# Kernel tuning notes

Measured on AMD Instinct MI355X. Metric: run time of the kernel, lower is better.

Reference implementation:

```python
import jax, jax.numpy as jnp
import numpy as np

B = 256
NUM_IN_CAPS = 1152   # 6*6*32
NUM_OUT_CAPS = 10
VEC_IN = 8
VEC_OUT = 16
ROUTING_ITERS = 3


def squash(x, axis):
    # squash(v) = |v|^2/(1+|v|^2) * v/|v|  (matches torch module, no eps)
    mag_squ = jnp.sum(x * x, axis=axis, keepdims=True)
    return mag_squ / (1.0 + mag_squ) * (x / jnp.sqrt(mag_squ))


def setup_inputs() -> dict:
    key = jax.random.key(0)
    k = jax.random.split(key, 6)
    x = jax.random.normal(k[0], (B, 1, 28, 28), dtype=jnp.float32)
    conv1_w = jax.random.normal(k[1], (256, 1, 9, 9), dtype=jnp.float32) * 0.1
    conv1_b = jnp.zeros((256,), dtype=jnp.float32)
    pc_w = jax.random.normal(k[2], (256, 256, 9, 9), dtype=jnp.float32) * 0.02  # out = 32 caps * 8 dims
    pc_b = jnp.zeros((256,), dtype=jnp.float32)
    # routing transform W: original shape [1,1152,160,8,1] -> [1152,10,16,8]
    W = jax.random.normal(k[3], (NUM_IN_CAPS, NUM_OUT_CAPS, VEC_OUT, VEC_IN), dtype=jnp.float32)
    dc_bias = jnp.zeros((NUM_OUT_CAPS, VEC_OUT), dtype=jnp.float32)
    return {"x": x, "conv1_w": conv1_w, "conv1_b": conv1_b,
            "pc_w": pc_w, "pc_b": pc_b, "W": W, "dc_bias": dc_bias}


def _conv(x, w, b, stride):
    y = jax.lax.conv_general_dilated(x, w, (stride, stride), 'VALID',
                                     dimension_numbers=('NCHW', 'OIHW', 'NCHW'))
    return y + b[None, :, None, None]


def reference(x, conv1_w, conv1_b, pc_w, pc_b, W, dc_bias):
    # conv1: [B,1,28,28] -> [B,256,20,20]  (no activation in original module)
    h = _conv(x, conv1_w, conv1_b, stride=1)
    # primaryCaps conv: -> [B,256,6,6] -> [B,1152,8]
    caps = _conv(h, pc_w, pc_b, stride=2)
    caps = caps.reshape(caps.shape[0], -1, VEC_IN)          # [B,1152,8]
    caps = squash(caps, axis=-1)
    # u_hat[b,i,j,d] = sum_k W[i,j,d,k] * caps[b,i,k]  (the original broadcast-mul-sum)
    u_hat = jnp.einsum('ijdk,bik->bijd', W, caps)           # [B,1152,10,16]
    b_ij = jnp.zeros(u_hat.shape[:3], dtype=u_hat.dtype)    # [B,1152,10]
    for r in range(ROUTING_ITERS):
        c_ij = jax.nn.softmax(b_ij, axis=2)                 # softmax over output caps
        s_j = jnp.einsum('bij,bijd->bjd', c_ij, u_hat) + dc_bias  # [B,10,16]
        v_j = squash(s_j, axis=-1)
        if r != ROUTING_ITERS - 1:
            b_ij = b_ij + jnp.einsum('bijd,bjd->bij', u_hat, v_j)
    return v_j  # [B,10,16]
```

## Files before the change

kernel.cpp:

```cpp
#include <hip/hip_runtime.h>
#include <hip/hip_bf16.h>


typedef __attribute__((ext_vector_type(8))) short short8;
typedef __attribute__((ext_vector_type(4))) float float4v;

__global__ __launch_bounds__(640) void conv1_kernel(const float* __restrict__ x,
    const float* __restrict__ w, const float* __restrict__ bias,
    __hip_bfloat16* __restrict__ ht){
  __shared__ float img[784];
  __shared__ float wsv[32 * 81];
  __shared__ ushort tile[400 * 33];
  int b = blockIdx.x;
  int og = blockIdx.y;
  int t = threadIdx.x;
  const float* xb = x + (size_t)b * 784;
  for (int idx = t; idx < 784; idx += 640) img[idx] = xb[idx];
  for (int idx = t; idx < 2592; idx += 640) wsv[idx] = w[(size_t)og * 2592 + idx];
  __syncthreads();
  int o_l = t / 20;
  int y   = t - o_l * 20;
  float acc[20];
  #pragma unroll
  for (int i = 0; i < 20; i++) acc[i] = 0.f;
  #pragma unroll
  for (int r = 0; r < 9; r++){
    float row[28];
    const float4* rp = (const float4*)&img[(y + r) * 28];
    #pragma unroll
    for (int q = 0; q < 7; q++){
      float4 v4 = rp[q];
      row[4*q+0]=v4.x; row[4*q+1]=v4.y; row[4*q+2]=v4.z; row[4*q+3]=v4.w;
    }
    #pragma unroll
    for (int s = 0; s < 9; s++){
      float wv = wsv[o_l * 81 + r * 9 + s];
      #pragma unroll
      for (int xx = 0; xx < 20; xx++)
        acc[xx] = fmaf(wv, row[xx + s], acc[xx]);
    }
  }
  float bv = bias[og * 32 + o_l];
  #pragma unroll
  for (int xx = 0; xx < 20; xx++){
    __hip_bfloat16 hv = __float2bfloat16(acc[xx] + bv);
    tile[(y * 20 + xx) * 33 + o_l] = *(ushort*)&hv;
  }
  __syncthreads();
  __hip_bfloat16* hb = ht + (size_t)b * 102400 + og * 32;
  for (int idx = t; idx < 6400; idx += 640){
    int pos = idx >> 4, op = idx & 15;
    unsigned v = (unsigned)tile[pos * 33 + op * 2]
               | ((unsigned)tile[pos * 33 + op * 2 + 1] << 16);
    *(unsigned*)(hb + (size_t)pos * 256 + op * 2) = v;
  }
}

__global__ __launch_bounds__(256) void arepack_kernel(const float* __restrict__ w2,
    ushort* __restrict__ A2s){
  __shared__ float wbuf[64 * 81];
  int o = blockIdx.x;
  int t = threadIdx.x;
  int ow = o >> 6, fo = (o >> 4) & 3, l15 = o & 15;
  size_t obase8 = (size_t)ow * 165888 + (size_t)fo * 64 + (size_t)l15 * 4;
  for (int c0 = 0; c0 < 256; c0 += 64){
    __syncthreads();
    for (int idx = t; idx < 5184; idx += 256)
      wbuf[idx] = w2[(size_t)o * 20736 + (size_t)c0 * 81 + idx];
    __syncthreads();
    for (int idx = t; idx < 2592; idx += 256){
      int rs = idx >> 5;
      int cp = (idx & 31) * 2;
      int cg = c0 + cp;
      int ct = cg >> 5, quad = (cg >> 3) & 3, e = cg & 7;
      __hip_bfloat16 b0 = __float2bfloat16(wbuf[cp * 81 + rs]);
      __hip_bfloat16 b1 = __float2bfloat16(wbuf[(cp + 1) * 81 + rs]);
      unsigned pack = (unsigned)*(ushort*)&b0 | ((unsigned)*(ushort*)&b1 << 16);
      size_t si = (obase8 + (size_t)ct * 256 + (size_t)rs * 2048 + quad) * 8 + e;
      *(unsigned*)(A2s + si) = pack;
    }
  }
}

__global__ __launch_bounds__(256, 2) void conv2_mfma_kernel(
    const __hip_bfloat16* __restrict__ ht, const short8* __restrict__ A2,
    float* __restrict__ caps4){
  __shared__ ushort img[2][400 * 40];
  int bx  = blockIdx.x;
  int xcd = bx & 7;
  int kq  = xcd >> 1;
  int p   = ((bx >> 3) << 1) | (xcd & 1);
  int b0  = p * 2;
  int t = threadIdx.x;
  int lane = t & 63;
  int wid  = t >> 6;
  int l15  = lane & 15;
  int quad = lane >> 4;

  int bn[3], slc[3];
  #pragma unroll
  for (int fn = 0; fn < 3; fn++){
    int n = fn * 16 + l15;
    int y = n / 6, xx = n - y * 6;
    if (n >= 36){ y = 0; xx = 0; }
    bn[fn]  = 40 * y + 2 * xx;
    slc[fn] = (quad + 4 * y) % 5;
  }
  const short8* i0p = (const short8*)&img[0][0];
  const short8* i1p = (const short8*)&img[1][0];

  float4v acc[4][6];
  #pragma unroll
  for (int fo = 0; fo < 4; fo++)
    #pragma unroll
    for (int fn = 0; fn < 6; fn++)
      acc[fo][fn] = (float4v){0.f, 0.f, 0.f, 0.f};

  for (int ci = 0; ci < 2; ci++){
    int ct = kq * 2 + ci;
    __syncthreads();
    #pragma unroll
    for (int im = 0; im < 2; im++){
      const __hip_bfloat16* hb = ht + (size_t)(b0 + im) * 102400;
      for (int idx = t; idx < 1600; idx += 256){
        int pp = idx >> 2, q = idx & 3;
        int sl = (q + 2 * (pp / 20)) % 5;
        uint4 v = *(const uint4*)(hb + (size_t)pp * 256 + ct * 32 + q * 8);
        *(uint4*)&img[im][pp * 40 + sl * 8] = v;
      }
    }
    __syncthreads();

    const short8* ap = A2 + ((size_t)wid * 648 + ct) * 256 + l15 * 4 + quad;

    short8 aF[2][4], bF[2][6];
    #pragma unroll
    for (int fo = 0; fo < 4; fo++) aF[0][fo] = ap[fo * 64];
    #pragma unroll
    for (int fn = 0; fn < 6; fn++){
      int f3 = (fn < 3) ? fn : fn - 3;
      const short8* ib = (fn < 3) ? i0p : i1p;
      bF[0][fn] = ib[bn[f3] * 5 + slc[f3]];
    }

    int rn = 0, sn = 0, r2m = 0;
    #pragma unroll 2
    for (int rs = 0; rs < 81; rs++){
      int cur = rs & 1, nxt = cur ^ 1;
      sn++;
      if (sn == 9){ sn = 0; rn++; r2m += 2; if (r2m >= 5) r2m -= 5; }
      int nrs = (rs < 80) ? rs + 1 : 80;
      int roff = rn * 20 + sn;
      const short8* apn = ap + (size_t)nrs * 2048;
      #pragma unroll
      for (int fo = 0; fo < 4; fo++) aF[nxt][fo] = apn[fo * 64];
      #pragma unroll
      for (int fn = 0; fn < 6; fn++){
        int f3 = (fn < 3) ? fn : fn - 3;
        const short8* ib = (fn < 3) ? i0p : i1p;
        int sl = slc[f3] + r2m; if (sl >= 5) sl -= 5;
        bF[nxt][fn] = ib[(bn[f3] + roff) * 5 + sl];
      }
      #pragma unroll
      for (int fo = 0; fo < 4; fo++)
        #pragma unroll
        for (int fn = 0; fn < 6; fn++)
          acc[fo][fn] = __builtin_amdgcn_mfma_f32_16x16x32_bf16(aF[cur][fo], bF[cur][fn], acc[fo][fn], 0, 0, 0);
    }
  }

  #pragma unroll
  for (int fn = 0; fn < 6; fn++){
    int im = (fn < 3) ? 0 : 1;
    int f3 = (fn < 3) ? fn : fn - 3;
    int pos = f3 * 16 + l15;
    if (pos < 36){
      float* cb = caps4 + ((size_t)kq * 256 + b0 + im) * 9216;
      #pragma unroll
      for (int fo = 0; fo < 4; fo++){
        int ob = wid * 64 + fo * 16 + quad * 4;
        #pragma unroll
        for (int rr = 0; rr < 4; rr++)
          cb[(size_t)(ob + rr) * 36 + pos] = acc[fo][fn][rr];
      }
    }
  }
}

__global__ __launch_bounds__(256) void squash4_kernel(const float* __restrict__ caps4,
    const float* __restrict__ bias, float* __restrict__ caps){
  size_t cid = (size_t)blockIdx.x * 256 + threadIdx.x;
  size_t base = cid * 8;
  const size_t STR = 2359296;
  float4 a0 = *(const float4*)(caps4 + base);
  float4 a1 = *(const float4*)(caps4 + base + 4);
  #pragma unroll
  for (int k = 1; k < 4; k++){
    float4 q0 = *(const float4*)(caps4 + k * STR + base);
    float4 q1 = *(const float4*)(caps4 + k * STR + base + 4);
    a0.x+=q0.x; a0.y+=q0.y; a0.z+=q0.z; a0.w+=q0.w;
    a1.x+=q1.x; a1.y+=q1.y; a1.z+=q1.z; a1.w+=q1.w;
  }
  int off = (int)(base % 9216);
  float v[8] = {a0.x,a0.y,a0.z,a0.w,a1.x,a1.y,a1.z,a1.w};
  #pragma unroll
  for (int e = 0; e < 8; e++) v[e] += bias[(off + e) / 36];
  float msq = 0.f;
  #pragma unroll
  for (int e = 0; e < 8; e++) msq += v[e]*v[e];
  float scale = sqrtf(msq) / (1.f + msq);
  float* cp = caps + base;
  #pragma unroll
  for (int e = 0; e < 8; e++) cp[e] = v[e]*scale;
}

__global__ __launch_bounds__(256) void uhat_kernel(const float* __restrict__ caps,
    const float* __restrict__ Wt, __hip_bfloat16* __restrict__ uh){
  __shared__ float cl[4096];
  int i0 = blockIdx.x * 32;
  int b0 = blockIdx.y * 16;
  int t = threadIdx.x;
  for (int idx = t; idx < 4096; idx += 256){
    int b_l = idx >> 8;
    int rest = idx & 255;
    cl[idx] = caps[((size_t)(b0 + b_l) * 1152 + i0 + (rest >> 3)) * 8 + (rest & 7)];
  }
  __syncthreads();
  int wid = t >> 6, l = t & 63;
  for (int ii = 0; ii < 8; ii++){
    int i = i0 + ii * 4 + wid;
    float wreg[3][8];
    #pragma unroll
    for (int m = 0; m < 3; m++){
      int jd = m * 64 + l;
      if (jd < 160){
        const float4* wp = (const float4*)&Wt[((size_t)i * 160 + jd) * 8];
        float4 p0 = wp[0], p1 = wp[1];
        wreg[m][0]=p0.x; wreg[m][1]=p0.y; wreg[m][2]=p0.z; wreg[m][3]=p0.w;
        wreg[m][4]=p1.x; wreg[m][5]=p1.y; wreg[m][6]=p1.z; wreg[m][7]=p1.w;
      }
    }
    for (int b_l = 0; b_l < 16; b_l++){
      const float4* cp4 = (const float4*)&cl[(b_l * 32 + ii * 4 + wid) * 8];
      float4 ca = cp4[0], cb = cp4[1];
      float ck[8] = {ca.x, ca.y, ca.z, ca.w, cb.x, cb.y, cb.z, cb.w};
      size_t ubase = ((size_t)(b0 + b_l) * 1152 + i) * 160;
      #pragma unroll
      for (int m = 0; m < 3; m++){
        int jd = m * 64 + l;
        if (jd < 160){
          float uv = 0.f;
          #pragma unroll
          for (int k = 0; k < 8; k++) uv = fmaf(wreg[m][k], ck[k], uv);
          uh[ubase + jd] = __float2bfloat16(uv);
        }
      }
    }
  }
}

__global__ __launch_bounds__(640, 2) void route_kernel(
    const __hip_bfloat16* __restrict__ u, const float* __restrict__ vin,
    const float* __restrict__ dcb, float* __restrict__ bbuf,
    float* __restrict__ vout, int mode){
  __shared__ float vs[160];
  __shared__ float dotb[320];
  __shared__ float cl[320];
  __shared__ float sp[4][160];
  int b = blockIdx.x;
  int t = threadIdx.x;
  int ipar = t / 160;
  int jd   = t - ipar * 160;
  int j    = jd >> 4;
  if (mode && t < 160) vs[t] = vin[b * 160 + t];
  __syncthreads();
  const __hip_bfloat16* ub = u + (size_t)b * 184320;
  float sacc = 0.f;
  for (int ch = 0; ch < 36; ch++){
    int ibase = ch * 32 + ipar * 8;
    float ureg[8];
    #pragma unroll
    for (int ii = 0; ii < 8; ii++)
      ureg[ii] = __bfloat162float(ub[(size_t)(ibase + ii) * 160 + jd]);
    if (mode){
      #pragma unroll
      for (int ii = 0; ii < 8; ii++){
        float pp = ureg[ii] * vs[jd];
        pp += __shfl_xor(pp, 1, 16);
        pp += __shfl_xor(pp, 2, 16);
        pp += __shfl_xor(pp, 4, 16);
        pp += __shfl_xor(pp, 8, 16);
        if ((jd & 15) == 0) dotb[(ipar * 8 + ii) * 10 + j] = pp;
      }
      __syncthreads();
      if (t < 320){
        float val = dotb[t];
        float* bg = bbuf + (size_t)b * 11520 + ch * 320 + t;
        if (mode == 2) val += *bg;
        else *bg = val;
        dotb[t] = val;
      }
      __syncthreads();
      if (t < 32){
        float dv[10]; float mx = -1e30f;
        #pragma unroll
        for (int q = 0; q < 10; q++){ dv[q] = dotb[t * 10 + q]; mx = fmaxf(mx, dv[q]); }
        float se = 0.f;
        #pragma unroll
        for (int q = 0; q < 10; q++){ dv[q] = __expf(dv[q] - mx); se += dv[q]; }
        float inv = 1.f / se;
        #pragma unroll
        for (int q = 0; q < 10; q++) cl[t * 10 + q] = dv[q] * inv;
      }
      __syncthreads();
      #pragma unroll
      for (int ii = 0; ii < 8; ii++)
        sacc = fmaf(cl[(ipar * 8 + ii) * 10 + j], ureg[ii], sacc);
    } else {
      #pragma unroll
      for (int ii = 0; ii < 8; ii++) sacc += ureg[ii];
    }
  }
  if (!mode) sacc *= 0.1f;
  sp[ipar][jd] = sacc;
  __syncthreads();
  if (t < 160){
    float sv = sp[0][t] + sp[1][t] + sp[2][t] + sp[3][t] + dcb[t];
    float msq = sv * sv;
    msq += __shfl_xor(msq, 1, 16);
    msq += __shfl_xor(msq, 2, 16);
    msq += __shfl_xor(msq, 4, 16);
    msq += __shfl_xor(msq, 8, 16);
    float scale = sqrtf(msq) / (1.f + msq);
    vout[b * 160 + t] = sv * scale;
  }
}

extern "C" void kernel_launch(void* const* d_in, const int* in_sizes, int n_in,
                              void* d_out, int out_size, void* d_ws, size_t ws_size,
                              hipStream_t stream){
  (void)in_sizes; (void)n_in; (void)out_size; (void)ws_size;
  const float* x   = (const float*)d_in[0];
  const float* w1  = (const float*)d_in[1];
  const float* b1  = (const float*)d_in[2];
  const float* w2  = (const float*)d_in[3];
  const float* b2  = (const float*)d_in[4];
  const float* W   = (const float*)d_in[5];
  const float* dcb = (const float*)d_in[6];
  float* out = (float*)d_out;

  char* ws = (char*)d_ws;
  __hip_bfloat16* ht  = (__hip_bfloat16*)(ws);
  ushort* A2s  = (ushort*)(ws + 52428800);
  float* caps4 = (float*)(ws + 63045632);
  __hip_bfloat16* uh = (__hip_bfloat16*)(ws);
  float* caps = (float*)(ws + 100794368);
  float* bbuf = (float*)(ws + 110231552);
  float* vbuf = (float*)(ws + 122028032);

  conv1_kernel<<<dim3(256, 8), 640, 0, stream>>>(x, w1, b1, ht);
  arepack_kernel<<<256, 256, 0, stream>>>(w2, A2s);
  conv2_mfma_kernel<<<512, 256, 0, stream>>>(ht, (const short8*)A2s, caps4);
  squash4_kernel<<<1152, 256, 0, stream>>>(caps4, b2, caps);
  uhat_kernel<<<dim3(36, 16), 256, 0, stream>>>(caps, W, uh);
  route_kernel<<<256, 640, 0, stream>>>(uh, vbuf, dcb, bbuf, vbuf, 0);
  route_kernel<<<256, 640, 0, stream>>>(uh, vbuf, dcb, bbuf, vbuf, 1);
  route_kernel<<<256, 640, 0, stream>>>(uh, vbuf, dcb, bbuf, out, 2);
}
```

Baseline: 473.6 us.

## Fuse three routing passes into one kernel with transposed u_hat layout

Replaces the three per-iteration routing launches with a single kernel per batch element that holds the routing logits in registers and the coupling coefficients in LDS. This removes the global bbuf and vbuf round trips and two launches. u_hat is now written in a transposed [b][jd][i] layout, and a new repack kernel transposes W so the u_hat kernel reads it coalesced. The fused kernel uses large LDS (about 50KB) and 576 threads with one block per batch element, which may limit occupancy.

```diff
diff --git a/kernel.cpp b/kernel.cpp
--- a/kernel.cpp
+++ b/kernel.cpp
@@ -4,6 +4,8 @@
 
 typedef __attribute__((ext_vector_type(8))) short short8;
 typedef __attribute__((ext_vector_type(4))) float float4v;
+
+__device__ inline float bfu(ushort v){ return __uint_as_float((unsigned)v << 16); }
 
 __global__ __launch_bounds__(640) void conv1_kernel(const float* __restrict__ x,
     const float* __restrict__ w, const float* __restrict__ bias,
@@ -82,6 +84,19 @@
   }
 }
 
+__global__ __launch_bounds__(256) void wrepack_kernel(const float* __restrict__ W,
+    float* __restrict__ Wr){
+  __shared__ float tile[64][65];
+  int r0 = blockIdx.x * 64;
+  int c0 = blockIdx.y * 64;
+  int t = threadIdx.x; int lx = t & 63, ly = t >> 6;
+  for (int rr = ly; rr < 64; rr += 4)
+    tile[rr][lx] = W[(size_t)(r0 + rr) * 1280 + c0 + lx];
+  __syncthreads();
+  for (int rr = ly; rr < 64; rr += 4)
+    Wr[(size_t)(c0 + rr) * 1152 + r0 + lx] = tile[lx][rr];
+}
+
 __global__ __launch_bounds__(256, 2) void conv2_mfma_kernel(
     const __hip_bfloat16* __restrict__ ht, const short8* __restrict__ A2,
     float* __restrict__ caps4){
@@ -214,125 +229,118 @@
   for (int e = 0; e < 8; e++) cp[e] = v[e]*scale;
 }
 
-__global__ __launch_bounds__(256) void uhat_kernel(const float* __restrict__ caps,
-    const float* __restrict__ Wt, __hip_bfloat16* __restrict__ uh){
-  __shared__ float cl[4096];
-  int i0 = blockIdx.x * 32;
-  int b0 = blockIdx.y * 16;
-  int t = threadIdx.x;
-  for (int idx = t; idx < 4096; idx += 256){
-    int b_l = idx >> 8;
-    int rest = idx & 255;
-    cl[idx] = caps[((size_t)(b0 + b_l) * 1152 + i0 + (rest >> 3)) * 8 + (rest & 7)];
+__global__ __launch_bounds__(256) void uhat_t_kernel(const float* __restrict__ caps,
+    const float* __restrict__ Wr, ushort* __restrict__ uT){
+  __shared__ float cl[8 * 8 * 64];
+  int i0 = blockIdx.x * 64;
+  int b0 = blockIdx.y * 8;
+  int t = threadIdx.x, lane = t & 63, w = t >> 6;
+  for (int f = t; f < 1024; f += 256){
+    int base = f * 4; int bb = base >> 9; int r = base & 511;
+    int il = r >> 3; int k = r & 7;
+    float4 v = *(const float4*)(caps + ((size_t)(b0+bb)*1152 + i0 + il)*8 + k);
+    cl[((k+0)*8+bb)*64+il] = v.x;
+    cl[((k+1)*8+bb)*64+il] = v.y;
+    cl[((k+2)*8+bb)*64+il] = v.z;
+    cl[((k+3)*8+bb)*64+il] = v.w;
   }
   __syncthreads();
-  int wid = t >> 6, l = t & 63;
-  for (int ii = 0; ii < 8; ii++){
-    int i = i0 + ii * 4 + wid;
-    float wreg[3][8];
-    #pragma unroll
-    for (int m = 0; m < 3; m++){
-      int jd = m * 64 + l;
-      if (jd < 160){
-        const float4* wp = (const float4*)&Wt[((size_t)i * 160 + jd) * 8];
-        float4 p0 = wp[0], p1 = wp[1];
-        wreg[m][0]=p0.x; wreg[m][1]=p0.y; wreg[m][2]=p0.z; wreg[m][3]=p0.w;
-        wreg[m][4]=p1.x; wreg[m][5]=p1.y; wreg[m][6]=p1.z; wreg[m][7]=p1.w;
-      }
-    }
-    for (int b_l = 0; b_l < 16; b_l++){
-      const float4* cp4 = (const float4*)&cl[(b_l * 32 + ii * 4 + wid) * 8];
-      float4 ca = cp4[0], cb = cp4[1];
-      float ck[8] = {ca.x, ca.y, ca.z, ca.w, cb.x, cb.y, cb.z, cb.w};
-      size_t ubase = ((size_t)(b0 + b_l) * 1152 + i) * 160;
-      #pragma unroll
-      for (int m = 0; m < 3; m++){
-        int jd = m * 64 + l;
-        if (jd < 160){
-          float uv = 0.f;
-          #pragma unroll
-          for (int k = 0; k < 8; k++) uv = fmaf(wreg[m][k], ck[k], uv);
-          uh[ubase + jd] = __float2bfloat16(uv);
-        }
-      }
-    }
-  }
-}
-
-__global__ __launch_bounds__(640, 2) void route_kernel(
-    const __hip_bfloat16* __restrict__ u, const float* __restrict__ vin,
-    const float* __restrict__ dcb, float* __restrict__ bbuf,
-    float* __restrict__ vout, int mode){
+  for (int jj = 0; jj < 40; jj++){
+    int jd = w * 40 + jj;
+    float wk[8];
+    #pragma unroll
+    for (int k = 0; k < 8; k++)
+      wk[k] = Wr[((size_t)jd * 8 + k) * 1152 + i0 + lane];
+    #pragma unroll
+    for (int bb = 0; bb < 8; bb++){
+      float acc = 0.f;
+      #pragma unroll
+      for (int k = 0; k < 8; k++) acc = fmaf(wk[k], cl[(k*8+bb)*64+lane], acc);
+      __hip_bfloat16 hv = __float2bfloat16(acc);
+      uT[((size_t)(b0+bb)*160 + jd)*1152 + i0 + lane] = *(ushort*)&hv;
+    }
+  }
+}
+
+__global__ __launch_bounds__(576) void route_fused_kernel(
+    const ushort* __restrict__ uT, const float* __restrict__ dcb,
+    float* __restrict__ out){
+  __shared__ float clds[1152 * 11];
+  __shared__ float s_lds[160];
   __shared__ float vs[160];
-  __shared__ float dotb[320];
-  __shared__ float cl[320];
-  __shared__ float sp[4][160];
   int b = blockIdx.x;
   int t = threadIdx.x;
-  int ipar = t / 160;
-  int jd   = t - ipar * 160;
-  int j    = jd >> 4;
-  if (mode && t < 160) vs[t] = vin[b * 160 + t];
-  __syncthreads();
-  const __hip_bfloat16* ub = u + (size_t)b * 184320;
-  float sacc = 0.f;
-  for (int ch = 0; ch < 36; ch++){
-    int ibase = ch * 32 + ipar * 8;
-    float ureg[8];
-    #pragma unroll
-    for (int ii = 0; ii < 8; ii++)
-      ureg[ii] = __bfloat162float(ub[(size_t)(ibase + ii) * 160 + jd]);
-    if (mode){
-      #pragma unroll
-      for (int ii = 0; ii < 8; ii++){
-        float pp = ureg[ii] * vs[jd];
-        pp += __shfl_xor(pp, 1, 16);
-        pp += __shfl_xor(pp, 2, 16);
-        pp += __shfl_xor(pp, 4, 16);
-        pp += __shfl_xor(pp, 8, 16);
-        if ((jd & 15) == 0) dotb[(ipar * 8 + ii) * 10 + j] = pp;
+  int lane = t & 63, w = t >> 6;
+  const ushort* ubT = uT + (size_t)b * 184320;
+  float breg[20];
+  #pragma unroll
+  for (int q = 0; q < 20; q++) breg[q] = 0.f;
+
+  for (int iter = 0; iter < 3; iter++){
+    if (iter){
+      #pragma unroll
+      for (int ih = 0; ih < 2; ih++){
+        int i = w * 128 + ih * 64 + lane;
+        const ushort* up = ubT + i;
+        float* bp = &breg[ih * 10];
+        #pragma unroll
+        for (int j = 0; j < 10; j++){
+          float dj = 0.f;
+          #pragma unroll
+          for (int d = 0; d < 16; d++){
+            int jd = j * 16 + d;
+            dj = fmaf(bfu(up[(size_t)jd * 1152]), vs[jd], dj);
+          }
+          bp[j] += dj;
+        }
+        float m = bp[0];
+        #pragma unroll
+        for (int j = 1; j < 10; j++) m = fmaxf(m, bp[j]);
+        float e[10], se = 0.f;
+        #pragma unroll
+        for (int j = 0; j < 10; j++){ e[j] = __expf(bp[j] - m); se += e[j]; }
+        float inv = 1.f / se;
+        #pragma unroll
+        for (int j = 0; j < 10; j++) clds[i * 11 + j] = e[j] * inv;
       }
       __syncthreads();
-      if (t < 320){
-        float val = dotb[t];
-        float* bg = bbuf + (size_t)b * 11520 + ch * 320 + t;
-        if (mode == 2) val += *bg;
-        else *bg = val;
-        dotb[t] = val;
-      }
-      __syncthreads();
-      if (t < 32){
-        float dv[10]; float mx = -1e30f;
-        #pragma unroll
-        for (int q = 0; q < 10; q++){ dv[q] = dotb[t * 10 + q]; mx = fmaxf(mx, dv[q]); }
-        float se = 0.f;
-        #pragma unroll
-        for (int q = 0; q < 10; q++){ dv[q] = __expf(dv[q] - mx); se += dv[q]; }
-        float inv = 1.f / se;
-        #pragma unroll
-        for (int q = 0; q < 10; q++) cl[t * 10 + q] = dv[q] * inv;
-      }
-      __syncthreads();
-      #pragma unroll
-      for (int ii = 0; ii < 8; ii++)
-        sacc = fmaf(cl[(ipar * 8 + ii) * 10 + j], ureg[ii], sacc);
-    } else {
-      #pragma unroll
-      for (int ii = 0; ii < 8; ii++) sacc += ureg[ii];
-    }
-  }
-  if (!mode) sacc *= 0.1f;
-  sp[ipar][jd] = sacc;
-  __syncthreads();
-  if (t < 160){
-    float sv = sp[0][t] + sp[1][t] + sp[2][t] + sp[3][t] + dcb[t];
-    float msq = sv * sv;
-    msq += __shfl_xor(msq, 1, 16);
-    msq += __shfl_xor(msq, 2, 16);
-    msq += __shfl_xor(msq, 4, 16);
-    msq += __shfl_xor(msq, 8, 16);
-    float scale = sqrtf(msq) / (1.f + msq);
-    vout[b * 160 + t] = sv * scale;
+    }
+    for (int jd = w; jd < 160; jd += 9){
+      const ushort* urow = ubT + (size_t)jd * 1152;
+      float sacc = 0.f;
+      if (iter == 0){
+        #pragma unroll
+        for (int st = 0; st < 18; st++)
+          sacc += bfu(urow[st * 64 + lane]);
+      } else {
+        int jj = jd >> 4;
+        #pragma unroll
+        for (int st = 0; st < 18; st++){
+          int i = st * 64 + lane;
+          sacc = fmaf(bfu(urow[i]), clds[i * 11 + jj], sacc);
+        }
+      }
+      sacc += __shfl_xor(sacc, 32);
+      sacc += __shfl_xor(sacc, 16);
+      sacc += __shfl_xor(sacc, 8);
+      sacc += __shfl_xor(sacc, 4);
+      sacc += __shfl_xor(sacc, 2);
+      sacc += __shfl_xor(sacc, 1);
+      if (lane == 0) s_lds[jd] = (iter == 0) ? sacc * 0.1f : sacc;
+    }
+    __syncthreads();
+    if (t < 160){
+      float sv = s_lds[t] + dcb[t];
+      float msq = sv * sv;
+      msq += __shfl_xor(msq, 1, 16);
+      msq += __shfl_xor(msq, 2, 16);
+      msq += __shfl_xor(msq, 4, 16);
+      msq += __shfl_xor(msq, 8, 16);
+      float scale = sqrtf(msq) / (1.f + msq);
+      if (iter == 2) out[b * 160 + t] = sv * scale;
+      else vs[t] = sv * scale;
+    }
+    __syncthreads();
   }
 }
 
@@ -350,20 +358,18 @@
   float* out = (float*)d_out;
 
   char* ws = (char*)d_ws;
-  __hip_bfloat16* ht  = (__hip_bfloat16*)(ws);
+  __hip_bfloat16* ht = (__hip_bfloat16*)(ws);
   ushort* A2s  = (ushort*)(ws + 52428800);
   float* caps4 = (float*)(ws + 63045632);
-  __hip_bfloat16* uh = (__hip_bfloat16*)(ws);
-  float* caps = (float*)(ws + 100794368);
-  float* bbuf = (float*)(ws + 110231552);
-  float* vbuf = (float*)(ws + 122028032);
+  ushort* uT   = (ushort*)(ws);
+  float* caps  = (float*)(ws + 100794368);
+  float* Wr    = (float*)(ws + 110231552);
 
   conv1_kernel<<<dim3(256, 8), 640, 0, stream>>>(x, w1, b1, ht);
   arepack_kernel<<<256, 256, 0, stream>>>(w2, A2s);
+  wrepack_kernel<<<dim3(18, 20), 256, 0, stream>>>(W, Wr);
   conv2_mfma_kernel<<<512, 256, 0, stream>>>(ht, (const short8*)A2s, caps4);
   squash4_kernel<<<1152, 256, 0, stream>>>(caps4, b2, caps);
-  uhat_kernel<<<dim3(36, 16), 256, 0, stream>>>(caps, W, uh);
-  route_kernel<<<256, 640, 0, stream>>>(uh, vbuf, dcb, bbuf, vbuf, 0);
-  route_kernel<<<256, 640, 0, stream>>>(uh, vbuf, dcb, bbuf, vbuf, 1);
-  route_kernel<<<256, 640, 0, stream>>>(uh, vbuf, dcb, bbuf, out, 2);
-}
+  uhat_t_kernel<<<dim3(18, 32), 256, 0, stream>>>(caps, Wr, uT);
+  route_fused_kernel<<<256, 576, 0, stream>>>(uT, dcb, out);
+}
```

After: 1.066 ms. +125.1%, slower.
